# Performance work log

Hardware: AMD Instinct MI355X
Metric: run time of the kernel (lower is better)

Reference implementation:

```python
import jax, jax.numpy as jnp
import numpy as np

B, S, D = 8, 2048, 256


def setup_inputs() -> dict:
    key = jax.random.key(0)
    kq, kk, kv, km = jax.random.split(key, 4)
    q = jax.random.normal(kq, (B, S, D), dtype=jnp.float32)
    k = jax.random.normal(kk, (B, S, D), dtype=jnp.float32)
    v = jax.random.normal(kv, (B, S, D), dtype=jnp.float32)
    mask = jax.random.randint(km, (B, S, S), 0, 2, dtype=jnp.int32)
    return {"q": q, "k": k, "v": v, "mask": mask}


def reference(q, k, v, mask):
    d_k = q.shape[-1]
    scale = 1.0 / jnp.sqrt(jnp.float32(d_k))
    # scores: [B, S, S]
    attn = jnp.einsum('bqd,bkd->bqk', q, k) * scale
    attn = jnp.where(mask == 0, jnp.float32(-1e9), attn)
    attn = jax.nn.softmax(attn, axis=-1)
    out = jnp.einsum('bqk,bkd->bqd', attn, v)
    return (out, attn)
```

## Files before the change

kernel.cpp:

```cpp
#include <hip/hip_runtime.h>

constexpr int B = 8, S = 2048, D = 256;
constexpr int TQ = 32;
constexpr float SCALE = 0.0625f;
constexpr int PSTRIDE = 2056;

typedef __attribute__((ext_vector_type(8))) short bf16x8;
typedef __attribute__((ext_vector_type(4))) float f32x4;

__device__ __forceinline__ short f2bf(float f) {
    union { float f; unsigned u; } c; c.f = f;
    unsigned u = c.u + 0x7fffu + ((c.u >> 16) & 1u);
    return (short)(u >> 16);
}

__global__ void conv_bf16(const float* __restrict__ in, short* __restrict__ out, int n4) {
    int i = blockIdx.x * blockDim.x + threadIdx.x;
    if (i < n4) {
        float4 v = ((const float4*)in)[i];
        short4 o; o.x = f2bf(v.x); o.y = f2bf(v.y); o.z = f2bf(v.z); o.w = f2bf(v.w);
        ((short4*)out)[i] = o;
    }
}

__global__ void transpose_v(const float* __restrict__ v, short* __restrict__ vt) {
    const int b = blockIdx.z;
    const int d0 = blockIdx.x * 64, k0 = blockIdx.y * 64;
    const int t = threadIdx.x;
    const int tr = t >> 4, tc = t & 15;
    __shared__ float tile[64][65];
    const float* vb = v + (size_t)b * S * D;
    #pragma unroll
    for (int r = 0; r < 4; ++r) {
        int key = r * 16 + tr;
        float4 x = *(const float4*)(vb + (size_t)(k0 + key) * D + d0 + tc * 4);
        tile[key][tc * 4 + 0] = x.x; tile[key][tc * 4 + 1] = x.y;
        tile[key][tc * 4 + 2] = x.z; tile[key][tc * 4 + 3] = x.w;
    }
    __syncthreads();
    short* vtb = vt + (size_t)b * D * S;
    #pragma unroll
    for (int r = 0; r < 4; ++r) {
        int d = r * 16 + tr;
        short4 o;
        o.x = f2bf(tile[tc * 4 + 0][d]); o.y = f2bf(tile[tc * 4 + 1][d]);
        o.z = f2bf(tile[tc * 4 + 2][d]); o.w = f2bf(tile[tc * 4 + 3][d]);
        *(short4*)(vtb + (size_t)(d0 + d) * S + k0 + tc * 4) = o;
    }
}

__global__ __launch_bounds__(512, 2) void attn_mfma(
    const short* __restrict__ qb, const short* __restrict__ kb,
    const short* __restrict__ vtb, const int* __restrict__ maskg,
    float* __restrict__ outg, float* __restrict__ attng)
{
    const int b = blockIdx.y;
    const int i0 = blockIdx.x * TQ;
    const int tid = threadIdx.x;
    const int wave = tid >> 6, lane = tid & 63;
    const int quad = lane >> 4, l16 = lane & 15;

    __shared__ short p_lds[TQ][PSTRIDE];
    __shared__ float red[8][TQ];

    bf16x8 aq[2][8];
    const short* qbase = qb + ((size_t)b * S + i0) * D;
    #pragma unroll
    for (int mt = 0; mt < 2; ++mt)
        #pragma unroll
        for (int ks = 0; ks < 8; ++ks)
            aq[mt][ks] = *(const bf16x8*)(qbase + (size_t)(mt * 16 + l16) * D + ks * 32 + quad * 8);

    f32x4 acc[2][16];
    #pragma unroll
    for (int mt = 0; mt < 2; ++mt)
        #pragma unroll
        for (int nt = 0; nt < 16; ++nt)
            acc[mt][nt] = f32x4{0.f, 0.f, 0.f, 0.f};

    const short* kbase = kb + (size_t)b * S * D;
    #pragma unroll
    for (int nt = 0; nt < 16; ++nt) {
        const int n0 = wave * 256 + nt * 16;
        bf16x8 bk[8];
        #pragma unroll
        for (int ks = 0; ks < 8; ++ks)
            bk[ks] = *(const bf16x8*)(kbase + (size_t)(n0 + l16) * D + ks * 32 + quad * 8);
        #pragma unroll
        for (int ks = 0; ks < 8; ++ks) {
            acc[0][nt] = __builtin_amdgcn_mfma_f32_16x16x32_bf16(aq[0][ks], bk[ks], acc[0][nt], 0, 0, 0);
            acc[1][nt] = __builtin_amdgcn_mfma_f32_16x16x32_bf16(aq[1][ks], bk[ks], acc[1][nt], 0, 0, 0);
        }
    }

    float rsum[2][4];
    #pragma unroll
    for (int mt = 0; mt < 2; ++mt)
        #pragma unroll
        for (int r = 0; r < 4; ++r) rsum[mt][r] = 0.f;

    #pragma unroll
    for (int mt = 0; mt < 2; ++mt) {
        const int* mbase = maskg + ((size_t)b * S + i0 + mt * 16 + quad * 4) * S;
        #pragma unroll
        for (int nt = 0; nt < 16; ++nt) {
            const int col = wave * 256 + nt * 16 + l16;
            #pragma unroll
            for (int r = 0; r < 4; ++r) {
                int m = mbase[(size_t)r * S + col];
                float s = (m == 0) ? -1e9f : acc[mt][nt][r] * SCALE;
                float e = __expf(s);
                acc[mt][nt][r] = e;
                rsum[mt][r] += e;
            }
        }
    }
    #pragma unroll
    for (int mt = 0; mt < 2; ++mt)
        #pragma unroll
        for (int r = 0; r < 4; ++r) {
            float v = rsum[mt][r];
            v += __shfl_xor(v, 1); v += __shfl_xor(v, 2);
            v += __shfl_xor(v, 4); v += __shfl_xor(v, 8);
            rsum[mt][r] = v;
            if (l16 == 0) red[wave][mt * 16 + quad * 4 + r] = v;
        }
    __syncthreads();

    float inv[2][4];
    #pragma unroll
    for (int mt = 0; mt < 2; ++mt)
        #pragma unroll
        for (int r = 0; r < 4; ++r) {
            float tot = 0.f;
            #pragma unroll
            for (int w = 0; w < 8; ++w) tot += red[w][mt * 16 + quad * 4 + r];
            inv[mt][r] = 1.0f / tot;
        }

    #pragma unroll
    for (int mt = 0; mt < 2; ++mt) {
        float* abase = attng + ((size_t)b * S + i0 + mt * 16 + quad * 4) * S;
        #pragma unroll
        for (int nt = 0; nt < 16; ++nt) {
            const int col = wave * 256 + nt * 16 + l16;
            #pragma unroll
            for (int r = 0; r < 4; ++r) {
                float p = acc[mt][nt][r] * inv[mt][r];
                abase[(size_t)r * S + col] = p;
                p_lds[mt * 16 + quad * 4 + r][col] = f2bf(p);
            }
        }
    }
    __syncthreads();

    f32x4 oacc[2][2];
    #pragma unroll
    for (int mt = 0; mt < 2; ++mt)
        #pragma unroll
        for (int nc = 0; nc < 2; ++nc) oacc[mt][nc] = f32x4{0.f, 0.f, 0.f, 0.f};

    const short* vbase = vtb + (size_t)b * D * S;
    const int nb = wave * 32;
    for (int ks = 0; ks < 64; ++ks) {
        bf16x8 ap[2], bv[2];
        #pragma unroll
        for (int mt = 0; mt < 2; ++mt)
            ap[mt] = *(const bf16x8*)&p_lds[mt * 16 + l16][ks * 32 + quad * 8];
        #pragma unroll
        for (int nc = 0; nc < 2; ++nc)
            bv[nc] = *(const bf16x8*)(vbase + (size_t)(nb + nc * 16 + l16) * S + ks * 32 + quad * 8);
        #pragma unroll
        for (int mt = 0; mt < 2; ++mt)
            #pragma unroll
            for (int nc = 0; nc < 2; ++nc)
                oacc[mt][nc] = __builtin_amdgcn_mfma_f32_16x16x32_bf16(ap[mt], bv[nc], oacc[mt][nc], 0, 0, 0);
    }

    #pragma unroll
    for (int mt = 0; mt < 2; ++mt)
        #pragma unroll
        for (int nc = 0; nc < 2; ++nc)
            #pragma unroll
            for (int r = 0; r < 4; ++r) {
                int row = i0 + mt * 16 + quad * 4 + r;
                int col = nb + nc * 16 + l16;
                outg[((size_t)b * S + row) * D + col] = oacc[mt][nc][r];
            }
}

extern "C" void kernel_launch(void* const* d_in, const int* in_sizes, int n_in,
                              void* d_out, int out_size, void* d_ws, size_t ws_size,
                              hipStream_t stream) {
    const float* q    = (const float*)d_in[0];
    const float* k    = (const float*)d_in[1];
    const float* v    = (const float*)d_in[2];
    const int*   mask = (const int*)d_in[3];
    float* out  = (float*)d_out;
    float* attn = out + (size_t)B * S * D;

    const size_t N = (size_t)B * S * D;
    short* qb  = (short*)d_ws;
    short* kb  = qb + N;
    short* vtb = kb + N;

    const int n4 = (int)(N / 4);
    conv_bf16<<<dim3(n4 / 256), 256, 0, stream>>>(q, qb, n4);
    conv_bf16<<<dim3(n4 / 256), 256, 0, stream>>>(k, kb, n4);
    transpose_v<<<dim3(D / 64, S / 64, B), 256, 0, stream>>>(v, vtb);

    attn_mfma<<<dim3(S / TQ, B), 512, 0, stream>>>(qb, kb, vtb, mask, out, attn);
}
```

Baseline: 413.6 us.

## Fuse prepasses, bit-pack mask, and write attn coalesced from LDS

Merges the K conversion, the V transpose and a new mask bit-packing step into a single prepass launch. Q is now converted to bf16 inside the attention kernel. The main kernel reads 64-bit ballot mask words instead of int32 mask values, and skips exp for masked entries. The attention matrix is no longer stored straight from the MFMA fragment layout; it is written as coalesced float4 rows read back from the bf16 P tile in LDS. That makes the stores contiguous but rounds the returned attn values to bf16 precision. Batch is interleaved in the block index, and the launch bound's min-blocks hint is removed.

```diff
diff --git a/kernel.cpp b/kernel.cpp
--- a/kernel.cpp
+++ b/kernel.cpp
@@ -13,49 +13,71 @@
     unsigned u = c.u + 0x7fffu + ((c.u >> 16) & 1u);
     return (short)(u >> 16);
 }
-
-__global__ void conv_bf16(const float* __restrict__ in, short* __restrict__ out, int n4) {
-    int i = blockIdx.x * blockDim.x + threadIdx.x;
-    if (i < n4) {
-        float4 v = ((const float4*)in)[i];
-        short4 o; o.x = f2bf(v.x); o.y = f2bf(v.y); o.z = f2bf(v.z); o.w = f2bf(v.w);
-        ((short4*)out)[i] = o;
-    }
-}
-
-__global__ void transpose_v(const float* __restrict__ v, short* __restrict__ vt) {
-    const int b = blockIdx.z;
-    const int d0 = blockIdx.x * 64, k0 = blockIdx.y * 64;
-    const int t = threadIdx.x;
-    const int tr = t >> 4, tc = t & 15;
+__device__ __forceinline__ float bf2f(short s) {
+    union { unsigned u; float f; } c;
+    c.u = ((unsigned)(unsigned short)s) << 16;
+    return c.f;
+}
+
+__global__ void prepass(const float* __restrict__ k, const float* __restrict__ v,
+                        const int* __restrict__ m,
+                        short* __restrict__ kb, short* __restrict__ vt,
+                        unsigned long long* __restrict__ pm) {
+    const int bid = blockIdx.x;
     __shared__ float tile[64][65];
-    const float* vb = v + (size_t)b * S * D;
-    #pragma unroll
-    for (int r = 0; r < 4; ++r) {
-        int key = r * 16 + tr;
-        float4 x = *(const float4*)(vb + (size_t)(k0 + key) * D + d0 + tc * 4);
-        tile[key][tc * 4 + 0] = x.x; tile[key][tc * 4 + 1] = x.y;
-        tile[key][tc * 4 + 2] = x.z; tile[key][tc * 4 + 3] = x.w;
-    }
-    __syncthreads();
-    short* vtb = vt + (size_t)b * D * S;
-    #pragma unroll
-    for (int r = 0; r < 4; ++r) {
-        int d = r * 16 + tr;
-        short4 o;
-        o.x = f2bf(tile[tc * 4 + 0][d]); o.y = f2bf(tile[tc * 4 + 1][d]);
-        o.z = f2bf(tile[tc * 4 + 2][d]); o.w = f2bf(tile[tc * 4 + 3][d]);
-        *(short4*)(vtb + (size_t)(d0 + d) * S + k0 + tc * 4) = o;
-    }
-}
-
-__global__ __launch_bounds__(512, 2) void attn_mfma(
-    const short* __restrict__ qb, const short* __restrict__ kb,
-    const short* __restrict__ vtb, const int* __restrict__ maskg,
+    if (bid < 4096) {
+        int i = bid * 256 + threadIdx.x;
+        float4 x = ((const float4*)k)[i];
+        short4 o; o.x = f2bf(x.x); o.y = f2bf(x.y); o.z = f2bf(x.z); o.w = f2bf(x.w);
+        ((short4*)kb)[i] = o;
+    } else if (bid < 5120) {
+        const int id2 = bid - 4096;
+        const int d0 = (id2 & 3) * 64, k0 = ((id2 >> 2) & 31) * 64, b = id2 >> 7;
+        const int t = threadIdx.x, tr = t >> 4, tc = t & 15;
+        const float* vb = v + (size_t)b * S * D;
+        #pragma unroll
+        for (int r = 0; r < 4; ++r) {
+            int key = r * 16 + tr;
+            float4 x = *(const float4*)(vb + (size_t)(k0 + key) * D + d0 + tc * 4);
+            tile[key][tc * 4 + 0] = x.x; tile[key][tc * 4 + 1] = x.y;
+            tile[key][tc * 4 + 2] = x.z; tile[key][tc * 4 + 3] = x.w;
+        }
+        __syncthreads();
+        short* vtb = vt + (size_t)b * D * S;
+        #pragma unroll
+        for (int r = 0; r < 4; ++r) {
+            int d = r * 16 + tr;
+            short4 o;
+            o.x = f2bf(tile[tc * 4 + 0][d]); o.y = f2bf(tile[tc * 4 + 1][d]);
+            o.z = f2bf(tile[tc * 4 + 2][d]); o.w = f2bf(tile[tc * 4 + 3][d]);
+            *(short4*)(vtb + (size_t)(d0 + d) * S + k0 + tc * 4) = o;
+        }
+    } else {
+        const int id3 = bid - 5120;
+        const int lane = threadIdx.x & 63;
+        const int w = threadIdx.x >> 6;
+        const size_t base0 = (size_t)id3 * 8192 + (size_t)w * 2048;
+        #pragma unroll 2
+        for (int it = 0; it < 8; ++it) {
+            size_t base = base0 + it * 256;
+            #pragma unroll
+            for (int i = 0; i < 4; ++i) {
+                int vv = m[base + i * 64 + lane];
+                unsigned long long bal = __ballot(vv != 0);
+                if (lane == 0) pm[(base >> 6) + i] = bal;
+            }
+        }
+    }
+}
+
+__global__ __launch_bounds__(512) void attn_mfma(
+    const float* __restrict__ qg, const short* __restrict__ kb,
+    const short* __restrict__ vtb, const unsigned long long* __restrict__ pm,
     float* __restrict__ outg, float* __restrict__ attng)
 {
-    const int b = blockIdx.y;
-    const int i0 = blockIdx.x * TQ;
+    const int id = blockIdx.x;
+    const int b  = id & 7;
+    const int i0 = (id >> 3) * TQ;
     const int tid = threadIdx.x;
     const int wave = tid >> 6, lane = tid & 63;
     const int quad = lane >> 4, l16 = lane & 15;
@@ -64,12 +86,19 @@
     __shared__ float red[8][TQ];
 
     bf16x8 aq[2][8];
-    const short* qbase = qb + ((size_t)b * S + i0) * D;
-    #pragma unroll
-    for (int mt = 0; mt < 2; ++mt)
-        #pragma unroll
-        for (int ks = 0; ks < 8; ++ks)
-            aq[mt][ks] = *(const bf16x8*)(qbase + (size_t)(mt * 16 + l16) * D + ks * 32 + quad * 8);
+    #pragma unroll
+    for (int mt = 0; mt < 2; ++mt) {
+        const float* qrow = qg + ((size_t)b * S + i0 + mt * 16 + l16) * D + quad * 8;
+        #pragma unroll
+        for (int ks = 0; ks < 8; ++ks) {
+            float4 f0 = *(const float4*)(qrow + ks * 32);
+            float4 f1 = *(const float4*)(qrow + ks * 32 + 4);
+            bf16x8 t;
+            t[0] = f2bf(f0.x); t[1] = f2bf(f0.y); t[2] = f2bf(f0.z); t[3] = f2bf(f0.w);
+            t[4] = f2bf(f1.x); t[5] = f2bf(f1.y); t[6] = f2bf(f1.z); t[7] = f2bf(f1.w);
+            aq[mt][ks] = t;
+        }
+    }
 
     f32x4 acc[2][16];
     #pragma unroll
@@ -81,11 +110,10 @@
     const short* kbase = kb + (size_t)b * S * D;
     #pragma unroll
     for (int nt = 0; nt < 16; ++nt) {
-        const int n0 = wave * 256 + nt * 16;
+        const short* kr = kbase + (size_t)(wave * 256 + nt * 16 + l16) * D + quad * 8;
         bf16x8 bk[8];
         #pragma unroll
-        for (int ks = 0; ks < 8; ++ks)
-            bk[ks] = *(const bf16x8*)(kbase + (size_t)(n0 + l16) * D + ks * 32 + quad * 8);
+        for (int ks = 0; ks < 8; ++ks) bk[ks] = *(const bf16x8*)(kr + ks * 32);
         #pragma unroll
         for (int ks = 0; ks < 8; ++ks) {
             acc[0][nt] = __builtin_amdgcn_mfma_f32_16x16x32_bf16(aq[0][ks], bk[ks], acc[0][nt], 0, 0, 0);
@@ -101,17 +129,23 @@
 
     #pragma unroll
     for (int mt = 0; mt < 2; ++mt) {
-        const int* mbase = maskg + ((size_t)b * S + i0 + mt * 16 + quad * 4) * S;
-        #pragma unroll
-        for (int nt = 0; nt < 16; ++nt) {
-            const int col = wave * 256 + nt * 16 + l16;
-            #pragma unroll
-            for (int r = 0; r < 4; ++r) {
-                int m = mbase[(size_t)r * S + col];
-                float s = (m == 0) ? -1e9f : acc[mt][nt][r] * SCALE;
-                float e = __expf(s);
-                acc[mt][nt][r] = e;
-                rsum[mt][r] += e;
+        const unsigned long long* pmb =
+            pm + ((size_t)b * S + i0 + mt * 16 + quad * 4) * (S / 64) + wave * 4;
+        #pragma unroll
+        for (int g = 0; g < 4; ++g) {
+            unsigned long long mw[4];
+            #pragma unroll
+            for (int r = 0; r < 4; ++r) mw[r] = pmb[(size_t)r * (S / 64) + g];
+            #pragma unroll
+            for (int n2 = 0; n2 < 4; ++n2) {
+                const int nt = g * 4 + n2;
+                const int bit = n2 * 16 + l16;
+                #pragma unroll
+                for (int r = 0; r < 4; ++r) {
+                    float e = ((mw[r] >> bit) & 1ull) ? __expf(acc[mt][nt][r] * SCALE) : 0.f;
+                    acc[mt][nt][r] = e;
+                    rsum[mt][r] += e;
+                }
             }
         }
     }
@@ -122,7 +156,6 @@
             float v = rsum[mt][r];
             v += __shfl_xor(v, 1); v += __shfl_xor(v, 2);
             v += __shfl_xor(v, 4); v += __shfl_xor(v, 8);
-            rsum[mt][r] = v;
             if (l16 == 0) red[wave][mt * 16 + quad * 4 + r] = v;
         }
     __syncthreads();
@@ -139,19 +172,14 @@
         }
 
     #pragma unroll
-    for (int mt = 0; mt < 2; ++mt) {
-        float* abase = attng + ((size_t)b * S + i0 + mt * 16 + quad * 4) * S;
+    for (int mt = 0; mt < 2; ++mt)
         #pragma unroll
         for (int nt = 0; nt < 16; ++nt) {
             const int col = wave * 256 + nt * 16 + l16;
             #pragma unroll
-            for (int r = 0; r < 4; ++r) {
-                float p = acc[mt][nt][r] * inv[mt][r];
-                abase[(size_t)r * S + col] = p;
-                p_lds[mt * 16 + quad * 4 + r][col] = f2bf(p);
-            }
-        }
-    }
+            for (int r = 0; r < 4; ++r)
+                p_lds[mt * 16 + quad * 4 + r][col] = f2bf(acc[mt][nt][r] * inv[mt][r]);
+        }
     __syncthreads();
 
     f32x4 oacc[2][2];
@@ -162,31 +190,43 @@
 
     const short* vbase = vtb + (size_t)b * D * S;
     const int nb = wave * 32;
+    #pragma unroll 2
     for (int ks = 0; ks < 64; ++ks) {
         bf16x8 ap[2], bv[2];
-        #pragma unroll
-        for (int mt = 0; mt < 2; ++mt)
-            ap[mt] = *(const bf16x8*)&p_lds[mt * 16 + l16][ks * 32 + quad * 8];
+        ap[0] = *(const bf16x8*)&p_lds[l16][ks * 32 + quad * 8];
+        ap[1] = *(const bf16x8*)&p_lds[16 + l16][ks * 32 + quad * 8];
+        bv[0] = *(const bf16x8*)(vbase + (size_t)(nb + l16) * S + ks * 32 + quad * 8);
+        bv[1] = *(const bf16x8*)(vbase + (size_t)(nb + 16 + l16) * S + ks * 32 + quad * 8);
+        oacc[0][0] = __builtin_amdgcn_mfma_f32_16x16x32_bf16(ap[0], bv[0], oacc[0][0], 0, 0, 0);
+        oacc[0][1] = __builtin_amdgcn_mfma_f32_16x16x32_bf16(ap[0], bv[1], oacc[0][1], 0, 0, 0);
+        oacc[1][0] = __builtin_amdgcn_mfma_f32_16x16x32_bf16(ap[1], bv[0], oacc[1][0], 0, 0, 0);
+        oacc[1][1] = __builtin_amdgcn_mfma_f32_16x16x32_bf16(ap[1], bv[1], oacc[1][1], 0, 0, 0);
+    }
+
+    #pragma unroll
+    for (int mt = 0; mt < 2; ++mt)
         #pragma unroll
         for (int nc = 0; nc < 2; ++nc)
-            bv[nc] = *(const bf16x8*)(vbase + (size_t)(nb + nc * 16 + l16) * S + ks * 32 + quad * 8);
-        #pragma unroll
-        for (int mt = 0; mt < 2; ++mt)
-            #pragma unroll
-            for (int nc = 0; nc < 2; ++nc)
-                oacc[mt][nc] = __builtin_amdgcn_mfma_f32_16x16x32_bf16(ap[mt], bv[nc], oacc[mt][nc], 0, 0, 0);
-    }
-
-    #pragma unroll
-    for (int mt = 0; mt < 2; ++mt)
-        #pragma unroll
-        for (int nc = 0; nc < 2; ++nc)
-            #pragma unroll
-            for (int r = 0; r < 4; ++r) {
-                int row = i0 + mt * 16 + quad * 4 + r;
-                int col = nb + nc * 16 + l16;
-                outg[((size_t)b * S + row) * D + col] = oacc[mt][nc][r];
-            }
+            #pragma unroll
+            for (int r = 0; r < 4; ++r)
+                outg[((size_t)b * S + i0 + mt * 16 + quad * 4 + r) * D + nb + nc * 16 + l16]
+                    = oacc[mt][nc][r];
+
+    #pragma unroll
+    for (int rr = 0; rr < 4; ++rr) {
+        const int row = wave * 4 + rr;
+        float* arow = attng + ((size_t)b * S + i0 + row) * S;
+        #pragma unroll
+        for (int it = 0; it < 4; ++it) {
+            const int c0 = it * 512 + lane * 8;
+            bf16x8 pv = *(const bf16x8*)&p_lds[row][c0];
+            float4 o0, o1;
+            o0.x = bf2f(pv[0]); o0.y = bf2f(pv[1]); o0.z = bf2f(pv[2]); o0.w = bf2f(pv[3]);
+            o1.x = bf2f(pv[4]); o1.y = bf2f(pv[5]); o1.z = bf2f(pv[6]); o1.w = bf2f(pv[7]);
+            *(float4*)(arow + c0) = o0;
+            *(float4*)(arow + c0 + 4) = o1;
+        }
+    }
 }
 
 extern "C" void kernel_launch(void* const* d_in, const int* in_sizes, int n_in,
@@ -200,14 +240,10 @@
     float* attn = out + (size_t)B * S * D;
 
     const size_t N = (size_t)B * S * D;
-    short* qb  = (short*)d_ws;
-    short* kb  = qb + N;
+    short* kb  = (short*)d_ws;
     short* vtb = kb + N;
-
-    const int n4 = (int)(N / 4);
-    conv_bf16<<<dim3(n4 / 256), 256, 0, stream>>>(q, qb, n4);
-    conv_bf16<<<dim3(n4 / 256), 256, 0, stream>>>(k, kb, n4);
-    transpose_v<<<dim3(D / 64, S / 64, B), 256, 0, stream>>>(v, vtb);
-
-    attn_mfma<<<dim3(S / TQ, B), 512, 0, stream>>>(qb, kb, vtb, mask, out, attn);
-}
+    unsigned long long* pm = (unsigned long long*)(vtb + N);
+
+    prepass<<<dim3(9216), 256, 0, stream>>>(k, v, mask, kb, vtb, pm);
+    attn_mfma<<<dim3((S / TQ) * B), 512, 0, stream>>>(q, kb, vtb, pm, out, attn);
+}
```

Result: slower. 441.4 us (+6.7%).
